# Kernel optimization log

Hardware: AMD Instinct MI355X
Metric: run time of the kernel (lower is better)

The kernel has to match this reference:

```python
import jax, jax.numpy as jnp
import numpy as np
from jax import lax

B, T_TOK, H, T_MEL, K = 32, 1024, 256, 4096, 5


def setup_inputs() -> dict:
    key = jax.random.key(0)
    ks = jax.random.split(key, 16)
    x = jax.random.normal(ks[0], (B, T_TOK, H), jnp.float32)
    token_nums = jax.random.randint(ks[1], (B,), T_TOK // 2, T_TOK)
    # ground-truth per-token durations in mel frames (avg ~4 frames/token)
    mels_alignations = jax.random.uniform(ks[2], (B, T_TOK), jnp.float32) * 8.0
    mels_gt_num = jax.random.randint(ks[3], (B,), T_MEL // 2, T_MEL)
    s = 1.0 / np.sqrt(H * K)
    conv1_w = jax.random.uniform(ks[4], (H, H, K), jnp.float32, -s, s)
    conv1_b = jax.random.uniform(ks[5], (H,), jnp.float32, -s, s)
    ln1_g = jnp.ones((H,), jnp.float32)
    ln1_b = jnp.zeros((H,), jnp.float32)
    conv2_w = jax.random.uniform(ks[6], (H, H, K), jnp.float32, -s, s)
    conv2_b = jax.random.uniform(ks[7], (H,), jnp.float32, -s, s)
    ln2_g = jnp.ones((H,), jnp.float32)
    ln2_b = jnp.zeros((H,), jnp.float32)
    sl = 1.0 / np.sqrt(H)
    lin_w = jax.random.uniform(ks[8], (1, H), jnp.float32, -sl, sl)
    lin_b = jax.random.uniform(ks[9], (1,), jnp.float32, -sl, sl)
    return {"x": x, "token_nums": token_nums, "mels_alignations": mels_alignations,
            "mels_gt_num": mels_gt_num, "conv1_w": conv1_w, "conv1_b": conv1_b,
            "ln1_g": ln1_g, "ln1_b": ln1_b, "conv2_w": conv2_w, "conv2_b": conv2_b,
            "ln2_g": ln2_g, "ln2_b": ln2_b, "lin_w": lin_w, "lin_b": lin_b}


def conv1d_same(x, w, b):
    # x: [B, T, H] -> conv over T with kernel [H_out, H_in, K], padding SAME
    y = lax.conv_general_dilated(x.transpose(0, 2, 1), w, (1,), 'SAME',
                                 dimension_numbers=('NCH', 'OIH', 'NCH'))
    return y.transpose(0, 2, 1) + b


def layer_norm(x, g, b, eps=1e-5):
    mu = jnp.mean(x, axis=-1, keepdims=True)
    var = jnp.mean(jnp.square(x - mu), axis=-1, keepdims=True)
    return (x - mu) * lax.rsqrt(var + eps) * g + b


def reference(x, token_nums, mels_alignations, mels_gt_num,
              conv1_w, conv1_b, ln1_g, ln1_b,
              conv2_w, conv2_b, ln2_g, ln2_b, lin_w, lin_b):
    # NOTE: original forward computes the conv1/ln1/relu1 branch then overwrites
    # m with conv2(x) -- the conv1 branch does not affect outputs, so it is skipped.
    m = conv1d_same(x, conv2_w, conv2_b)                 # [B, T_TOK, H]
    m = jax.nn.relu(layer_norm(m, ln2_g, ln2_b))
    m = (m @ lin_w.T + lin_b)[..., 0]                    # [B, T_TOK]
    mask = jnp.arange(T_TOK)[None, :] < token_nums[:, None]
    m = jnp.where(mask, m, 0.0)                          # mels_alignations_predicted
    exp_m = jnp.where(mask, jnp.exp(m), 0.0)
    mels_num_predicted = exp_m.sum(axis=1).astype(jnp.int32)

    # expansion: running-clipped cumsum of gt durations -> frame->token map
    cum = jnp.minimum(jnp.cumsum(mels_alignations, axis=1),
                      mels_gt_num[:, None].astype(jnp.float32))  # [B, T_TOK]
    frames = jnp.arange(T_MEL, dtype=jnp.float32)
    tok = jax.vmap(lambda c: jnp.searchsorted(c, frames, side='right'))(cum)  # [B, T_MEL]
    valid = tok < T_TOK
    tok_c = jnp.minimum(tok, T_TOK - 1)
    x_new = jnp.where(valid[:, :, None],
                      jnp.take_along_axis(x, tok_c[:, :, None], axis=1), 0.0)
    return x_new, m, mels_num_predicted
```

## Files before the change

### kernel.cpp

```cpp
#include <hip/hip_runtime.h>
#include <hip/hip_bf16.h>

#define B_SZ 32
#define T_TOK 1024
#define H_DIM 256
#define T_MEL 4096
#define K_SZ 5
#define BM 64
#define ROWS (BM + 4)
#define XS_BYTES (ROWS * 512)

typedef __attribute__((ext_vector_type(8))) short bf16x8;
typedef __attribute__((ext_vector_type(4))) float f32x4;

__device__ inline short f2bf(float f) {
    __hip_bfloat16 h = __float2bfloat16(f);
    return *reinterpret_cast<short*>(&h);
}

__global__ __launch_bounds__(256) void prep_kernel(const float* __restrict__ w,
                                                   short* __restrict__ wr,
                                                   const float* __restrict__ a,
                                                   const int* __restrict__ gt,
                                                   float* __restrict__ acc,
                                                   int* __restrict__ tokmap) {
    __shared__ float s_c[T_TOK];
    if (blockIdx.x < 160) {
        int idx = blockIdx.x * 256 + threadIdx.x;
        int lane = idx & 63;
        int n = (idx >> 6) & 15;
        int s = idx >> 10;
        int k = s >> 3;
        int hi0 = (s & 7) * 32 + (lane >> 4) * 8;
        int ho = n * 16 + (lane & 15);
        short out[8];
#pragma unroll
        for (int j = 0; j < 8; ++j)
            out[j] = f2bf(w[(ho * H_DIM + hi0 + j) * K_SZ + k]);
        *reinterpret_cast<bf16x8*>(wr + (size_t)idx * 8) = *reinterpret_cast<bf16x8*>(out);
        return;
    }
    int b = blockIdx.x - 160;
    int tid = threadIdx.x;
    if (tid == 1) acc[b] = 0.f;
    ((float4*)s_c)[tid] = ((const float4*)(a + b * T_TOK))[tid];
    __syncthreads();
    if (tid == 0) {
        float c = 0.f;
        float lim = (float)gt[b];
        for (int t = 0; t < T_TOK; ++t) {
            c += s_c[t];
            s_c[t] = fminf(c, lim);
        }
    }
    __syncthreads();
    int* tm = tokmap + b * T_MEL;
    for (int t = tid; t < T_TOK; t += 256) {
        float c1 = s_c[t];
        float c0 = (t == 0) ? 0.f : s_c[t - 1];
        int f0 = (int)ceilf(c0);
        int f1 = (int)ceilf(c1);
        for (int f = f0; f < f1; ++f) tm[f] = t;
    }
    int z0 = (int)ceilf(s_c[T_TOK - 1]);
    for (int f = z0 + tid; f < T_MEL; f += 256) tm[f] = T_TOK;
}

__global__ __launch_bounds__(512, 4) void fused_kernel(
    const float* __restrict__ x, const short* __restrict__ wr,
    const float* __restrict__ cb, const float* __restrict__ g,
    const float* __restrict__ beta, const float* __restrict__ lw,
    const float* __restrict__ lb, const int* __restrict__ tn,
    const int* __restrict__ tokmap,
    float* __restrict__ m_out, float* __restrict__ xnew, float* __restrict__ acc)
{
    __shared__ char smem[XS_BYTES + 6656];
    int tid = threadIdx.x;
    int lane = tid & 63;
    int wid = tid >> 6;
    int q = blockIdx.x / 3;
    int r = blockIdx.x % 3;

    if (r != 0) {
        int eidx = q * 2 + (r - 1);
        int fbase = eidx * 128;
        int b = eidx >> 5;
        int* s_tok = (int*)smem;
        if (tid < 128) s_tok[tid] = tokmap[fbase + tid];
        __syncthreads();
        const float* xb = x + (size_t)b * T_TOK * H_DIM;
        f32x4* dst = (f32x4*)(xnew + (size_t)(fbase + wid * 16) * H_DIM);
        f32x4 zv = {0.f, 0.f, 0.f, 0.f};
#pragma unroll
        for (int half = 0; half < 2; ++half) {
            f32x4 v[8];
#pragma unroll
            for (int i = 0; i < 8; ++i) {
                int tok = s_tok[wid * 16 + half * 8 + i];
                int tokc = min(tok, T_TOK - 1);
                v[i] = ((const f32x4*)(xb + (size_t)tokc * H_DIM))[lane];
                if (tok >= T_TOK) v[i] = zv;
            }
#pragma unroll
            for (int i = 0; i < 8; ++i)
                __builtin_nontemporal_store(v[i], dst + (half * 8 + i) * 64 + lane);
        }
        return;
    }

    int b = q >> 4;
    int t0 = (q & 15) * BM;

    for (int i = tid; i < ROWS * 64; i += 512) {
        int row = i >> 6;
        int c4 = i & 63;
        int t = t0 - 2 + row;
        float4 v = make_float4(0.f, 0.f, 0.f, 0.f);
        if (t >= 0 && t < T_TOK)
            v = *reinterpret_cast<const float4*>(x + ((size_t)b * T_TOK + t) * H_DIM + c4 * 4);
        short4 h;
        h.x = f2bf(v.x); h.y = f2bf(v.y); h.z = f2bf(v.z); h.w = f2bf(v.w);
        int byte = row * 512 + c4 * 8;
        byte ^= (row & 7) << 4;
        *reinterpret_cast<short4*>(smem + byte) = h;
    }
    __syncthreads();

    const bf16x8* wf = reinterpret_cast<const bf16x8*>(wr);
    f32x4 zero = {0.f, 0.f, 0.f, 0.f};
    f32x4 acc_[4][2];
#pragma unroll
    for (int mi = 0; mi < 4; ++mi)
#pragma unroll
        for (int ni = 0; ni < 2; ++ni) acc_[mi][ni] = zero;

    int arow = lane & 15;
    int ccol = (lane >> 4) * 16;
    int n16 = wid * 2;

    bf16x8 bc[2], bn[2];
#pragma unroll
    for (int ni = 0; ni < 2; ++ni) bc[ni] = wf[(size_t)(n16 + ni) * 64 + lane];

    for (int s = 0; s < 40; ++s) {
        if (s < 39) {
#pragma unroll
            for (int ni = 0; ni < 2; ++ni)
                bn[ni] = wf[(size_t)((s + 1) * 16 + n16 + ni) * 64 + lane];
        }
        int rb = arow + (s >> 3);
        int cbase = (s & 7) * 64 + ccol;
        bf16x8 a[4];
#pragma unroll
        for (int mi = 0; mi < 4; ++mi) {
            int rr = mi * 16 + rb;
            int by = (rr * 512 + cbase) ^ ((rr & 7) << 4);
            a[mi] = *reinterpret_cast<const bf16x8*>(smem + by);
        }
#pragma unroll
        for (int mi = 0; mi < 4; ++mi)
#pragma unroll
            for (int ni = 0; ni < 2; ++ni)
                acc_[mi][ni] = __builtin_amdgcn_mfma_f32_16x16x32_bf16(a[mi], bc[ni], acc_[mi][ni], 0, 0, 0);
#pragma unroll
        for (int ni = 0; ni < 2; ++ni) bc[ni] = bn[ni];
    }

    __syncthreads();
    float* ps   = reinterpret_cast<float*>(smem + XS_BYTES);
    float* pq   = ps + 512;
    float* pdot = pq + 512;
    float* mus  = pdot + 512;
    float* rss  = mus + 64;

    float cbv[2];
#pragma unroll
    for (int ni = 0; ni < 2; ++ni) cbv[ni] = cb[wid * 32 + ni * 16 + (lane & 15)];

#pragma unroll
    for (int mi = 0; mi < 4; ++mi)
#pragma unroll
        for (int rr = 0; rr < 4; ++rr) {
            float s = 0.f, qq = 0.f;
#pragma unroll
            for (int ni = 0; ni < 2; ++ni) {
                float v = acc_[mi][ni][rr] + cbv[ni];
                s += v; qq += v * v;
            }
#pragma unroll
            for (int m = 1; m < 16; m <<= 1) {
                s += __shfl_xor(s, m);
                qq += __shfl_xor(qq, m);
            }
            if ((lane & 15) == 0) {
                int row = mi * 16 + (lane >> 4) * 4 + rr;
                ps[row * 8 + wid] = s;
                pq[row * 8 + wid] = qq;
            }
        }
    __syncthreads();
    if (tid < 64) {
        float S = 0.f, Q = 0.f;
#pragma unroll
        for (int w = 0; w < 8; ++w) { S += ps[tid * 8 + w]; Q += pq[tid * 8 + w]; }
        float mu = S * (1.f / 256.f);
        float var = Q * (1.f / 256.f) - mu * mu;
        mus[tid] = mu;
        rss[tid] = rsqrtf(var + 1e-5f);
    }
    __syncthreads();

    float gv[2], bv[2], lv[2];
#pragma unroll
    for (int ni = 0; ni < 2; ++ni) {
        int col = wid * 32 + ni * 16 + (lane & 15);
        gv[ni] = g[col]; bv[ni] = beta[col]; lv[ni] = lw[col];
    }
#pragma unroll
    for (int mi = 0; mi < 4; ++mi)
#pragma unroll
        for (int rr = 0; rr < 4; ++rr) {
            int row = mi * 16 + (lane >> 4) * 4 + rr;
            float mu = mus[row], rs = rss[row];
            float dt = 0.f;
#pragma unroll
            for (int ni = 0; ni < 2; ++ni) {
                float v = acc_[mi][ni][rr] + cbv[ni];
                float y = fmaxf((v - mu) * rs * gv[ni] + bv[ni], 0.f);
                dt += y * lv[ni];
            }
#pragma unroll
            for (int m = 1; m < 16; m <<= 1) dt += __shfl_xor(dt, m);
            if ((lane & 15) == 0) pdot[row * 8 + wid] = dt;
        }
    __syncthreads();
    if (tid < 64) {
        float dot = lb[0];
#pragma unroll
        for (int w = 0; w < 8; ++w) dot += pdot[tid * 8 + w];
        int t = t0 + tid;
        float mv = (t < tn[b]) ? dot : 0.f;
        m_out[b * T_TOK + t] = mv;
        float e = (t < tn[b]) ? expf(mv) : 0.f;
#pragma unroll
        for (int m = 1; m < 64; m <<= 1) e += __shfl_xor(e, m);
        if (tid == 0) atomicAdd(&acc[b], e);
    }
}

__global__ __launch_bounds__(64) void finalize_kernel(const float* __restrict__ acc,
                                                      float* __restrict__ out) {
    int b = threadIdx.x;
    if (b < B_SZ) out[b] = (float)((int)acc[b]);
}

extern "C" void kernel_launch(void* const* d_in, const int* in_sizes, int n_in,
                              void* d_out, int out_size, void* d_ws, size_t ws_size,
                              hipStream_t stream) {
    const float* x          = (const float*)d_in[0];
    const int*   token_nums = (const int*)d_in[1];
    const float* align      = (const float*)d_in[2];
    const int*   gt         = (const int*)d_in[3];
    const float* w2  = (const float*)d_in[8];
    const float* b2  = (const float*)d_in[9];
    const float* g2  = (const float*)d_in[10];
    const float* be2 = (const float*)d_in[11];
    const float* lw  = (const float*)d_in[12];
    const float* lb  = (const float*)d_in[13];

    float* out   = (float*)d_out;
    float* xnew  = out;
    float* m_out = out + (size_t)B_SZ * T_MEL * H_DIM;
    float* mels  = m_out + (size_t)B_SZ * T_TOK;

    short* wr   = (short*)d_ws;
    float* acc  = (float*)((char*)d_ws + (size_t)40 * 16 * 64 * 8 * 2);
    int* tokmap = (int*)((char*)acc + 128);

    prep_kernel<<<192, 256, 0, stream>>>(w2, wr, align, gt, acc, tokmap);
    fused_kernel<<<1536, 512, 0, stream>>>(x, wr, b2, g2, be2, lw, lb,
                                           token_nums, tokmap, m_out, xnew, acc);
    finalize_kernel<<<1, 64, 0, stream>>>(acc, mels);
}
```

Measured before the change: 79.69 us.

## Use persistent blocks with atomic work queue and fuse finalize into main kernel

```diff
diff --git a/kernel.cpp b/kernel.cpp
--- a/kernel.cpp
+++ b/kernel.cpp
@@ -9,6 +9,9 @@
 #define BM 64
 #define ROWS (BM + 4)
 #define XS_BYTES (ROWS * 512)
+#define NCONV 512
+#define NEXP 1024
+#define NUNITS (NCONV + NEXP)
 
 typedef __attribute__((ext_vector_type(8))) short bf16x8;
 typedef __attribute__((ext_vector_type(4))) float f32x4;
@@ -23,7 +26,8 @@
                                                    const float* __restrict__ a,
                                                    const int* __restrict__ gt,
                                                    float* __restrict__ acc,
-                                                   int* __restrict__ tokmap) {
+                                                   int* __restrict__ tokmap,
+                                                   int* __restrict__ ctrs) {
     __shared__ float s_c[T_TOK];
     if (blockIdx.x < 160) {
         int idx = blockIdx.x * 256 + threadIdx.x;
@@ -43,6 +47,7 @@
     int b = blockIdx.x - 160;
     int tid = threadIdx.x;
     if (tid == 1) acc[b] = 0.f;
+    if (b == 0 && tid == 2) { ctrs[0] = 0; ctrs[1] = 0; }
     ((float4*)s_c)[tid] = ((const float4*)(a + b * T_TOK))[tid];
     __syncthreads();
     if (tid == 0) {
@@ -72,186 +77,198 @@
     const float* __restrict__ beta, const float* __restrict__ lw,
     const float* __restrict__ lb, const int* __restrict__ tn,
     const int* __restrict__ tokmap,
-    float* __restrict__ m_out, float* __restrict__ xnew, float* __restrict__ acc)
+    float* __restrict__ m_out, float* __restrict__ xnew, float* __restrict__ acc,
+    int* __restrict__ ctrs, float* __restrict__ mels)
 {
-    __shared__ char smem[XS_BYTES + 6656];
+    __shared__ char smem[XS_BYTES];
+    __shared__ int s_unit;
     int tid = threadIdx.x;
     int lane = tid & 63;
     int wid = tid >> 6;
-    int q = blockIdx.x / 3;
-    int r = blockIdx.x % 3;
-
-    if (r != 0) {
-        int eidx = q * 2 + (r - 1);
-        int fbase = eidx * 128;
-        int b = eidx >> 5;
-        int* s_tok = (int*)smem;
-        if (tid < 128) s_tok[tid] = tokmap[fbase + tid];
-        __syncthreads();
-        const float* xb = x + (size_t)b * T_TOK * H_DIM;
-        f32x4* dst = (f32x4*)(xnew + (size_t)(fbase + wid * 16) * H_DIM);
-        f32x4 zv = {0.f, 0.f, 0.f, 0.f};
-#pragma unroll
-        for (int half = 0; half < 2; ++half) {
-            f32x4 v[8];
-#pragma unroll
-            for (int i = 0; i < 8; ++i) {
-                int tok = s_tok[wid * 16 + half * 8 + i];
-                int tokc = min(tok, T_TOK - 1);
-                v[i] = ((const f32x4*)(xb + (size_t)tokc * H_DIM))[lane];
-                if (tok >= T_TOK) v[i] = zv;
-            }
-#pragma unroll
-            for (int i = 0; i < 8; ++i)
-                __builtin_nontemporal_store(v[i], dst + (half * 8 + i) * 64 + lane);
-        }
-        return;
-    }
-
-    int b = q >> 4;
-    int t0 = (q & 15) * BM;
-
-    for (int i = tid; i < ROWS * 64; i += 512) {
-        int row = i >> 6;
-        int c4 = i & 63;
-        int t = t0 - 2 + row;
-        float4 v = make_float4(0.f, 0.f, 0.f, 0.f);
-        if (t >= 0 && t < T_TOK)
-            v = *reinterpret_cast<const float4*>(x + ((size_t)b * T_TOK + t) * H_DIM + c4 * 4);
-        short4 h;
-        h.x = f2bf(v.x); h.y = f2bf(v.y); h.z = f2bf(v.z); h.w = f2bf(v.w);
-        int byte = row * 512 + c4 * 8;
-        byte ^= (row & 7) << 4;
-        *reinterpret_cast<short4*>(smem + byte) = h;
-    }
-    __syncthreads();
-
-    const bf16x8* wf = reinterpret_cast<const bf16x8*>(wr);
-    f32x4 zero = {0.f, 0.f, 0.f, 0.f};
-    f32x4 acc_[4][2];
-#pragma unroll
-    for (int mi = 0; mi < 4; ++mi)
-#pragma unroll
-        for (int ni = 0; ni < 2; ++ni) acc_[mi][ni] = zero;
-
-    int arow = lane & 15;
-    int ccol = (lane >> 4) * 16;
-    int n16 = wid * 2;
-
-    bf16x8 bc[2], bn[2];
-#pragma unroll
-    for (int ni = 0; ni < 2; ++ni) bc[ni] = wf[(size_t)(n16 + ni) * 64 + lane];
-
-    for (int s = 0; s < 40; ++s) {
-        if (s < 39) {
-#pragma unroll
-            for (int ni = 0; ni < 2; ++ni)
-                bn[ni] = wf[(size_t)((s + 1) * 16 + n16 + ni) * 64 + lane];
-        }
-        int rb = arow + (s >> 3);
-        int cbase = (s & 7) * 64 + ccol;
-        bf16x8 a[4];
-#pragma unroll
-        for (int mi = 0; mi < 4; ++mi) {
-            int rr = mi * 16 + rb;
-            int by = (rr * 512 + cbase) ^ ((rr & 7) << 4);
-            a[mi] = *reinterpret_cast<const bf16x8*>(smem + by);
-        }
+
+    for (;;) {
+        __syncthreads();
+        if (tid == 0) s_unit = atomicAdd(&ctrs[0], 1);
+        __syncthreads();
+        int u = s_unit;
+        if (u >= NUNITS) break;
+
+        if (u >= NCONV) {
+            int e = u - NCONV;
+            int fbase = e * 128;
+            int b = e >> 5;
+            int* s_tok = (int*)smem;
+            if (tid < 128) s_tok[tid] = tokmap[fbase + tid];
+            __syncthreads();
+            const float* xb = x + (size_t)b * T_TOK * H_DIM;
+            f32x4* dst = (f32x4*)(xnew + (size_t)(fbase + wid * 16) * H_DIM);
+            f32x4 zv = {0.f, 0.f, 0.f, 0.f};
+#pragma unroll
+            for (int half = 0; half < 2; ++half) {
+                f32x4 v[8];
+#pragma unroll
+                for (int i = 0; i < 8; ++i) {
+                    int tok = s_tok[wid * 16 + half * 8 + i];
+                    int tokc = min(tok, T_TOK - 1);
+                    v[i] = ((const f32x4*)(xb + (size_t)tokc * H_DIM))[lane];
+                    if (tok >= T_TOK) v[i] = zv;
+                }
+#pragma unroll
+                for (int i = 0; i < 8; ++i)
+                    __builtin_nontemporal_store(v[i], dst + (half * 8 + i) * 64 + lane);
+            }
+            continue;
+        }
+
+        int b = u >> 4;
+        int t0 = (u & 15) * BM;
+
+        for (int i = tid; i < ROWS * 64; i += 512) {
+            int row = i >> 6;
+            int c4 = i & 63;
+            int t = t0 - 2 + row;
+            float4 v = make_float4(0.f, 0.f, 0.f, 0.f);
+            if (t >= 0 && t < T_TOK)
+                v = *reinterpret_cast<const float4*>(x + ((size_t)b * T_TOK + t) * H_DIM + c4 * 4);
+            short4 h;
+            h.x = f2bf(v.x); h.y = f2bf(v.y); h.z = f2bf(v.z); h.w = f2bf(v.w);
+            int byte = row * 512 + c4 * 8;
+            byte ^= (row & 7) << 4;
+            *reinterpret_cast<short4*>(smem + byte) = h;
+        }
+        __syncthreads();
+
+        const bf16x8* wf = reinterpret_cast<const bf16x8*>(wr);
+        f32x4 zero = {0.f, 0.f, 0.f, 0.f};
+        f32x4 acc_[4][2];
 #pragma unroll
         for (int mi = 0; mi < 4; ++mi)
 #pragma unroll
-            for (int ni = 0; ni < 2; ++ni)
-                acc_[mi][ni] = __builtin_amdgcn_mfma_f32_16x16x32_bf16(a[mi], bc[ni], acc_[mi][ni], 0, 0, 0);
-#pragma unroll
-        for (int ni = 0; ni < 2; ++ni) bc[ni] = bn[ni];
-    }
-
-    __syncthreads();
-    float* ps   = reinterpret_cast<float*>(smem + XS_BYTES);
-    float* pq   = ps + 512;
-    float* pdot = pq + 512;
-    float* mus  = pdot + 512;
-    float* rss  = mus + 64;
-
-    float cbv[2];
-#pragma unroll
-    for (int ni = 0; ni < 2; ++ni) cbv[ni] = cb[wid * 32 + ni * 16 + (lane & 15)];
-
-#pragma unroll
-    for (int mi = 0; mi < 4; ++mi)
-#pragma unroll
-        for (int rr = 0; rr < 4; ++rr) {
-            float s = 0.f, qq = 0.f;
-#pragma unroll
-            for (int ni = 0; ni < 2; ++ni) {
-                float v = acc_[mi][ni][rr] + cbv[ni];
-                s += v; qq += v * v;
-            }
-#pragma unroll
-            for (int m = 1; m < 16; m <<= 1) {
-                s += __shfl_xor(s, m);
-                qq += __shfl_xor(qq, m);
-            }
-            if ((lane & 15) == 0) {
+            for (int ni = 0; ni < 2; ++ni) acc_[mi][ni] = zero;
+
+        int arow = lane & 15;
+        int ccol = (lane >> 4) * 16;
+        int n16 = wid * 2;
+
+        bf16x8 bc[2], bn[2];
+#pragma unroll
+        for (int ni = 0; ni < 2; ++ni) bc[ni] = wf[(size_t)(n16 + ni) * 64 + lane];
+
+        for (int s = 0; s < 40; ++s) {
+            if (s < 39) {
+#pragma unroll
+                for (int ni = 0; ni < 2; ++ni)
+                    bn[ni] = wf[(size_t)((s + 1) * 16 + n16 + ni) * 64 + lane];
+            }
+            int rb = arow + (s >> 3);
+            int cbase = (s & 7) * 64 + ccol;
+            bf16x8 a[4];
+#pragma unroll
+            for (int mi = 0; mi < 4; ++mi) {
+                int rr = mi * 16 + rb;
+                int by = (rr * 512 + cbase) ^ ((rr & 7) << 4);
+                a[mi] = *reinterpret_cast<const bf16x8*>(smem + by);
+            }
+#pragma unroll
+            for (int mi = 0; mi < 4; ++mi)
+#pragma unroll
+                for (int ni = 0; ni < 2; ++ni)
+                    acc_[mi][ni] = __builtin_amdgcn_mfma_f32_16x16x32_bf16(a[mi], bc[ni], acc_[mi][ni], 0, 0, 0);
+#pragma unroll
+            for (int ni = 0; ni < 2; ++ni) bc[ni] = bn[ni];
+        }
+
+        __syncthreads();
+        float* ps   = reinterpret_cast<float*>(smem);
+        float* pq   = ps + 512;
+        float* pdot = pq + 512;
+        float* mus  = pdot + 512;
+        float* rss  = mus + 64;
+
+        float cbv[2];
+#pragma unroll
+        for (int ni = 0; ni < 2; ++ni) cbv[ni] = cb[wid * 32 + ni * 16 + (lane & 15)];
+
+#pragma unroll
+        for (int mi = 0; mi < 4; ++mi)
+#pragma unroll
+            for (int rr = 0; rr < 4; ++rr) {
+                float s = 0.f, qq = 0.f;
+#pragma unroll
+                for (int ni = 0; ni < 2; ++ni) {
+                    float v = acc_[mi][ni][rr] + cbv[ni];
+                    s += v; qq += v * v;
+                }
+#pragma unroll
+                for (int m = 1; m < 16; m <<= 1) {
+                    s += __shfl_xor(s, m);
+                    qq += __shfl_xor(qq, m);
+                }
+                if ((lane & 15) == 0) {
+                    int row = mi * 16 + (lane >> 4) * 4 + rr;
+                    ps[row * 8 + wid] = s;
+                    pq[row * 8 + wid] = qq;
+                }
+            }
+        __syncthreads();
+        if (tid < 64) {
+            float S = 0.f, Q = 0.f;
+#pragma unroll
+            for (int w = 0; w < 8; ++w) { S += ps[tid * 8 + w]; Q += pq[tid * 8 + w]; }
+            float mu = S * (1.f / 256.f);
+            float var = Q * (1.f / 256.f) - mu * mu;
+            mus[tid] = mu;
+            rss[tid] = rsqrtf(var + 1e-5f);
+        }
+        __syncthreads();
+
+        float gv[2], bv[2], lv[2];
+#pragma unroll
+        for (int ni = 0; ni < 2; ++ni) {
+            int col = wid * 32 + ni * 16 + (lane & 15);
+            gv[ni] = g[col]; bv[ni] = beta[col]; lv[ni] = lw[col];
+        }
+#pragma unroll
+        for (int mi = 0; mi < 4; ++mi)
+#pragma unroll
+            for (int rr = 0; rr < 4; ++rr) {
                 int row = mi * 16 + (lane >> 4) * 4 + rr;
-                ps[row * 8 + wid] = s;
-                pq[row * 8 + wid] = qq;
-            }
-        }
-    __syncthreads();
-    if (tid < 64) {
-        float S = 0.f, Q = 0.f;
-#pragma unroll
-        for (int w = 0; w < 8; ++w) { S += ps[tid * 8 + w]; Q += pq[tid * 8 + w]; }
-        float mu = S * (1.f / 256.f);
-        float var = Q * (1.f / 256.f) - mu * mu;
-        mus[tid] = mu;
-        rss[tid] = rsqrtf(var + 1e-5f);
-    }
-    __syncthreads();
-
-    float gv[2], bv[2], lv[2];
-#pragma unroll
-    for (int ni = 0; ni < 2; ++ni) {
-        int col = wid * 32 + ni * 16 + (lane & 15);
-        gv[ni] = g[col]; bv[ni] = beta[col]; lv[ni] = lw[col];
-    }
-#pragma unroll
-    for (int mi = 0; mi < 4; ++mi)
-#pragma unroll
-        for (int rr = 0; rr < 4; ++rr) {
-            int row = mi * 16 + (lane >> 4) * 4 + rr;
-            float mu = mus[row], rs = rss[row];
-            float dt = 0.f;
-#pragma unroll
-            for (int ni = 0; ni < 2; ++ni) {
-                float v = acc_[mi][ni][rr] + cbv[ni];
-                float y = fmaxf((v - mu) * rs * gv[ni] + bv[ni], 0.f);
-                dt += y * lv[ni];
-            }
-#pragma unroll
-            for (int m = 1; m < 16; m <<= 1) dt += __shfl_xor(dt, m);
-            if ((lane & 15) == 0) pdot[row * 8 + wid] = dt;
-        }
-    __syncthreads();
-    if (tid < 64) {
-        float dot = lb[0];
-#pragma unroll
-        for (int w = 0; w < 8; ++w) dot += pdot[tid * 8 + w];
-        int t = t0 + tid;
-        float mv = (t < tn[b]) ? dot : 0.f;
-        m_out[b * T_TOK + t] = mv;
-        float e = (t < tn[b]) ? expf(mv) : 0.f;
-#pragma unroll
-        for (int m = 1; m < 64; m <<= 1) e += __shfl_xor(e, m);
-        if (tid == 0) atomicAdd(&acc[b], e);
-    }
-}
-
-__global__ __launch_bounds__(64) void finalize_kernel(const float* __restrict__ acc,
-                                                      float* __restrict__ out) {
-    int b = threadIdx.x;
-    if (b < B_SZ) out[b] = (float)((int)acc[b]);
+                float mu = mus[row], rs = rss[row];
+                float dt = 0.f;
+#pragma unroll
+                for (int ni = 0; ni < 2; ++ni) {
+                    float v = acc_[mi][ni][rr] + cbv[ni];
+                    float y = fmaxf((v - mu) * rs * gv[ni] + bv[ni], 0.f);
+                    dt += y * lv[ni];
+                }
+#pragma unroll
+                for (int m = 1; m < 16; m <<= 1) dt += __shfl_xor(dt, m);
+                if ((lane & 15) == 0) pdot[row * 8 + wid] = dt;
+            }
+        __syncthreads();
+        if (tid < 64) {
+            float dot = lb[0];
+#pragma unroll
+            for (int w = 0; w < 8; ++w) dot += pdot[tid * 8 + w];
+            int t = t0 + tid;
+            float mv = (t < tn[b]) ? dot : 0.f;
+            m_out[b * T_TOK + t] = mv;
+            float e = (t < tn[b]) ? expf(mv) : 0.f;
+#pragma unroll
+            for (int m = 1; m < 64; m <<= 1) e += __shfl_xor(e, m);
+            if (tid == 0) atomicAdd(&acc[b], e);
+        }
+    }
+
+    __threadfence();
+    if (tid == 0) {
+        if (atomicAdd(&ctrs[1], 1) == (int)gridDim.x - 1) {
+            for (int b = 0; b < B_SZ; ++b) {
+                float v = atomicAdd(&acc[b], 0.f);
+                mels[b] = (float)((int)v);
+            }
+        }
+    }
 }
 
 extern "C" void kernel_launch(void* const* d_in, const int* in_sizes, int n_in,
@@ -276,9 +293,10 @@
     short* wr   = (short*)d_ws;
     float* acc  = (float*)((char*)d_ws + (size_t)40 * 16 * 64 * 8 * 2);
     int* tokmap = (int*)((char*)acc + 128);
-
-    prep_kernel<<<192, 256, 0, stream>>>(w2, wr, align, gt, acc, tokmap);
-    fused_kernel<<<1536, 512, 0, stream>>>(x, wr, b2, g2, be2, lw, lb,
-                                           token_nums, tokmap, m_out, xnew, acc);
-    finalize_kernel<<<1, 64, 0, stream>>>(acc, mels);
+    int* ctrs   = (int*)((char*)tokmap + (size_t)B_SZ * T_MEL * 4);
+
+    prep_kernel<<<192, 256, 0, stream>>>(w2, wr, align, gt, acc, tokmap, ctrs);
+    fused_kernel<<<1024, 512, 0, stream>>>(x, wr, b2, g2, be2, lw, lb,
+                                           token_nums, tokmap, m_out, xnew, acc,
+                                           ctrs, mels);
 }
```

Result: slower. 267.8 us (+236.0%).
